# Optimization experiments

Measured on AMD Instinct MI355X. Metric: run time of the kernel, lower is better.

Reference implementation:

```python
import jax, jax.numpy as jnp
import numpy as np

B, T, K, D = 32, 1000, 512, 512


def setup_inputs() -> dict:
    key = jax.random.key(0)
    ks = jax.random.split(key, 10)
    s = lambda k, shape: jax.random.normal(k, shape, jnp.float32) * 0.05
    return {
        "zi": jax.random.randint(ks[0], (B, T), 0, K),
        "c": jax.random.normal(ks[1], (B, D, T), jnp.float32),
        "emb": s(ks[2], (K, D)),
        "W1": s(ks[3], (2 * D, D)), "b1": jnp.zeros((D,), jnp.float32),
        "W2": s(ks[4], (D, D)), "b2": jnp.zeros((D,), jnp.float32),
        "W_ih": s(ks[5], (D, 4 * D)), "b_ih": jnp.zeros((4 * D,), jnp.float32),
        "W_hh": s(ks[6], (D, 4 * D)), "b_hh": jnp.zeros((4 * D,), jnp.float32),
        "W_out": s(ks[7], (D, K)), "b_out": jnp.zeros((K,), jnp.float32),
    }


def reference(zi, c, emb, W1, b1, W2, b2, W_ih, b_ih, W_hh, b_hh, W_out, b_out):
    Bb, Tt = zi.shape
    Dd = emb.shape[1]
    # teacher-forced inputs: embed and shift right by one (pad with zeros)
    z = emb[zi]                                                    # [B,T,D]
    z_prev = jnp.concatenate([jnp.zeros((Bb, 1, Dd), z.dtype), z[:, :-1]], axis=1)
    x = jnp.concatenate([z_prev, jnp.transpose(c, (0, 2, 1))], axis=-1)  # [B,T,2D]
    # prenet has no sequential dependence -> batch over all timesteps
    pre = jax.nn.relu(x @ W1 + b1) @ W2 + b2                       # [B,T,D]
    # precompute the input-to-hidden gate contribution for all steps
    xg = jnp.transpose(pre @ W_ih + b_ih + b_hh, (1, 0, 2))        # [T,B,4D]

    def step(carry, gx):
        h, cc = carry
        gates = gx + h @ W_hh                                      # [B,4D]
        i, f, g, o = jnp.split(gates, 4, axis=-1)                  # torch LSTMCell order
        i = jax.nn.sigmoid(i)
        f = jax.nn.sigmoid(f)
        g = jnp.tanh(g)
        o = jax.nn.sigmoid(o)
        cc = f * cc + i * g
        h = o * jnp.tanh(cc)
        return (h, cc), h

    h0 = jnp.zeros((Bb, Dd), pre.dtype)
    _, hs = jax.lax.scan(step, (h0, h0), xg)                       # [T,B,D]
    logits = hs @ W_out + b_out                                    # [T,B,K]
    return jnp.transpose(logits, (1, 2, 0))                        # [B,K,T]
```

## Files before the change

kernel.cpp:

```cpp
#include <hip/hip_runtime.h>
#include <stdint.h>

typedef unsigned short u16;
typedef unsigned int u32;
typedef unsigned long long u64;
typedef __attribute__((ext_vector_type(8))) short bh8;
typedef __attribute__((ext_vector_type(8))) unsigned short u16x8;
typedef __attribute__((ext_vector_type(4))) float f32x4;

#define B_ 32
#define T_ 1000
#define D_ 512
#define NG 2048

__device__ __forceinline__ float bf2f(u16 u) {
  union { unsigned int i; float f; } v; v.i = ((unsigned int)u) << 16; return v.f;
}
__device__ __forceinline__ u16 f2bf(float f) {
  union { float f; unsigned int i; } v; v.f = f;
  return (u16)((v.i + 0x7fffu + ((v.i >> 16) & 1u)) >> 16);
}

__global__ __launch_bounds__(256) void wtrans_k(const float* __restrict__ src,
                                                u16* __restrict__ dst, int R, int C) {
  __shared__ float tile[32][33];
  const int r0 = blockIdx.x * 32, c0 = blockIdx.y * 32;
  const int tid = threadIdx.x;
#pragma unroll
  for (int q = 0; q < 4; q++) {
    int idx = q * 256 + tid, rr = idx >> 5, cc = idx & 31;
    tile[rr][cc] = src[(size_t)(r0 + rr) * C + c0 + cc];
  }
  __syncthreads();
#pragma unroll
  for (int q = 0; q < 4; q++) {
    int idx = q * 256 + tid, cc = idx >> 5, rr = idx & 31;
    dst[(size_t)(c0 + cc) * R + r0 + rr] = f2bf(tile[rr][cc]);
  }
}

__global__ void bsum_k(const float* __restrict__ a, const float* __restrict__ b,
                       float* __restrict__ o) {
  int i = blockIdx.x * blockDim.x + threadIdx.x;
  if (i < NG) o[i] = a[i] + b[i];
}

__global__ __launch_bounds__(256) void embed_k(const int* __restrict__ zi,
                                               const float* __restrict__ emb,
                                               u16* __restrict__ x) {
  const int tid = threadIdx.x;
  const int r = blockIdx.x * 4 + (tid >> 6);
  const int d0 = (tid & 63) * 8;
  const int t = r >> 5, b = r & 31;
  u16x8 o;
  if (t == 0) {
#pragma unroll
    for (int i = 0; i < 8; i++) o[i] = 0;
  } else {
    const int zv = zi[b * T_ + t - 1];
    const float* s = emb + (size_t)zv * D_ + d0;
#pragma unroll
    for (int i = 0; i < 8; i++) o[i] = f2bf(s[i]);
  }
  *(u16x8*)(x + (size_t)r * 1024 + d0) = o;
}

__global__ __launch_bounds__(256) void ctrans_k(const float* __restrict__ c,
                                                u16* __restrict__ x) {
  __shared__ float tile[32][65];
  const int b = blockIdx.z, d0 = blockIdx.y * 32, t0 = blockIdx.x * 64;
  const int tid = threadIdx.x;
  const int dd = tid >> 3, tt0 = (tid & 7) * 8;
  const float* src = c + ((size_t)b * D_ + d0 + dd) * T_ + t0 + tt0;
#pragma unroll
  for (int i = 0; i < 8; i++) {
    int tt = tt0 + i;
    tile[dd][tt] = (t0 + tt < T_) ? src[i] : 0.f;
  }
  __syncthreads();
  const int tt = tid & 63, dq = tid >> 6;
  if (t0 + tt < T_) {
    u16x8 o;
#pragma unroll
    for (int i = 0; i < 8; i++) o[i] = f2bf(tile[dq * 8 + i][tt]);
    *(u16x8*)(x + ((size_t)(t0 + tt) * 32 + b) * 1024 + 512 + d0 + dq * 8) = o;
  }
}

template <bool RELU, bool SCATTER>
__global__ __launch_bounds__(256, 2) void gemm_k(const u16* __restrict__ A,
                                                 const u16* __restrict__ Bt,
                                                 const float* __restrict__ bias,
                                                 void* __restrict__ Cout,
                                                 int M, int N, int K) {
  __shared__ u16 Al[128 * 40];
  __shared__ u16 Bl[128 * 40];
  const int tid = threadIdx.x;
  const int w = tid >> 6, l = tid & 63;
  const int row0 = blockIdx.x * 128, col0 = blockIdx.y * 128;
  const int wr = (w >> 1) * 64, wc = (w & 1) * 64;
  f32x4 acc[4][4];
  const f32x4 zero = {0.f, 0.f, 0.f, 0.f};
#pragma unroll
  for (int i = 0; i < 4; i++)
#pragma unroll
    for (int j = 0; j < 4; j++) acc[i][j] = zero;

  const int sm = tid >> 2;
  const int sk = (tid & 3) * 8;
  const u16* Ap = A + (size_t)(row0 + sm) * K + sk;
  const u16* Bp = Bt + (size_t)(col0 + sm) * K + sk;
  const size_t half = (size_t)64 * K;
  const int ldo = sm * 40 + sk;
  const int lr = l & 15, lk = (l >> 4) * 8;
  const int KT = K >> 5;

  bh8 a0 = *(const bh8*)Ap, a1 = *(const bh8*)(Ap + half);
  bh8 b0 = *(const bh8*)Bp, b1 = *(const bh8*)(Bp + half);

  for (int kt = 0; kt < KT; kt++) {
    const int kn = (kt + 1 < KT) ? (kt + 1) * 32 : 0;
    bh8 na0 = *(const bh8*)(Ap + kn), na1 = *(const bh8*)(Ap + half + kn);
    bh8 nb0 = *(const bh8*)(Bp + kn), nb1 = *(const bh8*)(Bp + half + kn);
    *(bh8*)(Al + ldo) = a0;
    *(bh8*)(Al + ldo + 64 * 40) = a1;
    *(bh8*)(Bl + ldo) = b0;
    *(bh8*)(Bl + ldo + 64 * 40) = b1;
    __syncthreads();
    bh8 af[4], bfr[4];
#pragma unroll
    for (int i = 0; i < 4; i++) af[i] = *(const bh8*)(Al + (wr + i * 16 + lr) * 40 + lk);
#pragma unroll
    for (int j = 0; j < 4; j++) bfr[j] = *(const bh8*)(Bl + (wc + j * 16 + lr) * 40 + lk);
#pragma unroll
    for (int i = 0; i < 4; i++)
#pragma unroll
      for (int j = 0; j < 4; j++)
        acc[i][j] = __builtin_amdgcn_mfma_f32_16x16x32_bf16(af[i], bfr[j], acc[i][j], 0, 0, 0);
    __syncthreads();
    a0 = na0; a1 = na1; b0 = nb0; b1 = nb1;
  }

  const int lrow = (l >> 4) * 4;
#pragma unroll
  for (int j = 0; j < 4; j++) {
    const int n = col0 + wc + j * 16 + lr;
    const float bv = bias[n];
#pragma unroll
    for (int i = 0; i < 4; i++) {
      const int r = row0 + wr + i * 16 + lrow;
      if (SCATTER) {
        const int bb = r / T_;
        const int t = r - bb * T_;
        f32x4 o;
#pragma unroll
        for (int e = 0; e < 4; e++) o[e] = acc[i][j][e] + bv;
        *(f32x4*)((float*)Cout + ((size_t)bb * N + n) * T_ + t) = o;
      } else {
#pragma unroll
        for (int e = 0; e < 4; e++) {
          float v = acc[i][j][e] + bv;
          if (RELU) v = v > 0.f ? v : 0.f;
          ((u16*)Cout)[(size_t)(r + e) * N + n] = f2bf(v);
        }
      }
    }
  }
}

__device__ __forceinline__ void poll8(const u32* p, u64 q[8], bool slow) {
  const u64 a = (u64)(uintptr_t)p;
  if (!slow) {
    asm volatile(
        "global_load_dwordx2 %0, %8, off sc0\n\t"
        "global_load_dwordx2 %1, %8, off offset:256 sc0\n\t"
        "global_load_dwordx2 %2, %8, off offset:512 sc0\n\t"
        "global_load_dwordx2 %3, %8, off offset:768 sc0\n\t"
        "global_load_dwordx2 %4, %8, off offset:1024 sc0\n\t"
        "global_load_dwordx2 %5, %8, off offset:1280 sc0\n\t"
        "global_load_dwordx2 %6, %8, off offset:1536 sc0\n\t"
        "global_load_dwordx2 %7, %8, off offset:1792 sc0\n\t"
        "s_waitcnt vmcnt(0)"
        : "=&v"(q[0]), "=&v"(q[1]), "=&v"(q[2]), "=&v"(q[3]),
          "=&v"(q[4]), "=&v"(q[5]), "=&v"(q[6]), "=&v"(q[7])
        : "v"(a)
        : "memory");
  } else {
    asm volatile(
        "global_load_dwordx2 %0, %8, off sc1\n\t"
        "global_load_dwordx2 %1, %8, off offset:256 sc1\n\t"
        "global_load_dwordx2 %2, %8, off offset:512 sc1\n\t"
        "global_load_dwordx2 %3, %8, off offset:768 sc1\n\t"
        "global_load_dwordx2 %4, %8, off offset:1024 sc1\n\t"
        "global_load_dwordx2 %5, %8, off offset:1280 sc1\n\t"
        "global_load_dwordx2 %6, %8, off offset:1536 sc1\n\t"
        "global_load_dwordx2 %7, %8, off offset:1792 sc1\n\t"
        "s_waitcnt vmcnt(0)"
        : "=&v"(q[0]), "=&v"(q[1]), "=&v"(q[2]), "=&v"(q[3]),
          "=&v"(q[4]), "=&v"(q[5]), "=&v"(q[6]), "=&v"(q[7])
        : "v"(a)
        : "memory");
  }
}

__global__ __launch_bounds__(256, 1) void scan_k(const u16* __restrict__ xg,
                                                 const u16* __restrict__ Whht,
                                                 u16* __restrict__ hs,
                                                 u32* hbuf) {
  __shared__ u16 hstage[16 * 512];
  __shared__ float gl[4][68];
  const int tid = threadIdx.x;
  const int wgid = blockIdx.x;
  const int grp = wgid & 7;
  const int wgin = wgid >> 3;
  const int D0 = wgin * 16;
  const int w = tid >> 6, l = tid & 63;
  const int lr = l & 15, lc = l >> 4;

  u32* fb = hbuf;
  u32* sb = hbuf + 32768;

  bh8 bfr[16];
  {
    const u16* wp = Whht + (size_t)(w * 512 + D0 + lr) * 512 + lc * 8;
#pragma unroll
    for (int kk = 0; kk < 16; kk++) bfr[kk] = *(const bh8*)(wp + kk * 32);
  }

  for (int i = tid; i < 16 * 256; i += 256) ((u32*)hstage)[i] = 0u;

  const int pb = l >> 4, pd = l & 15;
  const int gbat = grp * 4 + pb;
  float ccv = 0.f;
  u16 xh[4];
  if (w == 0) {
    const u16* xp = xg + (size_t)gbat * NG + D0 + pd;
#pragma unroll
    for (int g = 0; g < 4; g++) xh[g] = xp[g * 512];
  }
  const int rb = (w - 2) * 2 + (l >> 5);
  const int l5 = l & 31;
  bool slowmode = false;
  __syncthreads();

  for (int t = 0; t < T_; t++) {
    f32x4 e0 = {0.f, 0.f, 0.f, 0.f}, e1 = e0;
#pragma unroll
    for (int kk = 0; kk < 16; kk += 2) {
      bh8 af0 = *(const bh8*)(hstage + (kk + 0) * 512 + l * 8);
      bh8 af1 = *(const bh8*)(hstage + (kk + 1) * 512 + l * 8);
      e0 = __builtin_amdgcn_mfma_f32_16x16x32_bf16(af0, bfr[kk + 0], e0, 0, 0, 0);
      e1 = __builtin_amdgcn_mfma_f32_16x16x32_bf16(af1, bfr[kk + 1], e1, 0, 0, 0);
    }
    const f32x4 acc = e0 + e1;
    if (lc == 0) {
#pragma unroll
      for (int e = 0; e < 4; e++) gl[e][w * 16 + lr] = acc[e];
    }
    asm volatile("s_waitcnt lgkmcnt(0)\n\ts_barrier" ::: "memory");
    __builtin_amdgcn_sched_barrier(0);

    if (w == 0) {
      const float gi = gl[pb][ 0 + pd] + bf2f(xh[0]);
      const float gf = gl[pb][16 + pd] + bf2f(xh[1]);
      const float gg = gl[pb][32 + pd] + bf2f(xh[2]);
      const float go = gl[pb][48 + pd] + bf2f(xh[3]);
      const float si = 1.f / (1.f + __expf(-gi));
      const float sf = 1.f / (1.f + __expf(-gf));
      const float tg = 1.f - 2.f / (__expf(2.f * gg) + 1.f);
      const float so = 1.f / (1.f + __expf(-go));
      ccv = sf * ccv + si * tg;
      const float hv = so * (1.f - 2.f / (__expf(2.f * ccv) + 1.f));
      const u16 hb = f2bf(hv);
      if (t + 1 < T_) {
        const u32 tagged = ((u32)(t + 1) << 16) | (u32)hb;
        const size_t idx = ((size_t)((t & 1) * 8 + grp) * 4 + pb) * 512 + D0 + pd;
        asm volatile("global_store_dword %0, %1, off sc0"
                     :: "v"((u64)(uintptr_t)(fb + idx)), "v"(tagged) : "memory");
        (void)__hip_atomic_exchange(sb + idx, tagged, __ATOMIC_RELAXED,
                                    __HIP_MEMORY_SCOPE_AGENT);
      }
      hs[((size_t)gbat * T_ + t) * 512 + D0 + pd] = hb;
      if (t + 1 < T_) {
        const u16* xp = xg + ((size_t)(t + 1) * 32 + gbat) * NG + D0 + pd;
#pragma unroll
        for (int g = 0; g < 4; g++) xh[g] = xp[g * 512];
      }
    } else if (w >= 2 && t + 1 < T_) {
      const u32 tag = (u32)(t + 1);
      const size_t base = ((size_t)((t & 1) * 8 + grp) * 4 + rb) * 512 + 2 * l5;
      u64 q[8];
      int rounds = 0;
      for (;;) {
        poll8(fb + base, q, false);
        if (slowmode) poll8(sb + base, q, true);
        u32 bad = 0;
#pragma unroll
        for (int s = 0; s < 8; s++) {
          bad |= ((u32)q[s] >> 16) ^ tag;
          bad |= ((u32)(q[s] >> 32) >> 16) ^ tag;
        }
        if (!__ballot(bad != 0u)) break;
        if (++rounds > 256) slowmode = true;
      }
#pragma unroll
      for (int s = 0; s < 8; s++) {
        const int k = 2 * l5 + 64 * s;
        const u32 wv = ((u32)q[s] & 0xffffu) | ((u32)(q[s] >> 32) << 16);
        *(u32*)(hstage + (k >> 5) * 512 + (rb + ((k >> 3) & 3) * 16) * 8 + (k & 7)) = wv;
      }
    }
    asm volatile("s_waitcnt lgkmcnt(0)\n\ts_barrier" ::: "memory");
    __builtin_amdgcn_sched_barrier(0);
  }
}

extern "C" void kernel_launch(void* const* d_in, const int* in_sizes, int n_in,
                              void* d_out, int out_size, void* d_ws, size_t ws_size,
                              hipStream_t stream) {
  const int*   zi    = (const int*)d_in[0];
  const float* c     = (const float*)d_in[1];
  const float* emb   = (const float*)d_in[2];
  const float* W1    = (const float*)d_in[3];
  const float* b1    = (const float*)d_in[4];
  const float* W2    = (const float*)d_in[5];
  const float* b2    = (const float*)d_in[6];
  const float* W_ih  = (const float*)d_in[7];
  const float* b_ih  = (const float*)d_in[8];
  const float* W_hh  = (const float*)d_in[9];
  const float* b_hh  = (const float*)d_in[10];
  const float* W_out = (const float*)d_in[11];
  const float* b_out = (const float*)d_in[12];
  float* out = (float*)d_out;
  char* ws = (char*)d_ws;

  const size_t x_off   = 0;
  const size_t xg_off  = 65536000;
  const size_t pre_off = 32768000;
  const size_t w_off   = xg_off + 131072000;
  u16* xb    = (u16*)(ws + x_off);
  u16* hsb   = (u16*)(ws + x_off);
  u16* preb  = (u16*)(ws + pre_off);
  u16* xgb   = (u16*)(ws + xg_off);
  u16* h1b   = (u16*)(ws + xg_off);
  u16* W1t   = (u16*)(ws + w_off);
  u16* W2t   = W1t + 512 * 1024;
  u16* Wiht  = W2t + 512 * 512;
  u16* Whht  = Wiht + 2048 * 512;
  u16* Woutt = Whht + 2048 * 512;
  float* bsum = (float*)(Woutt + 512 * 512);
  u32* hbuf  = (u32*)(bsum + NG);

  hipMemsetAsync(hbuf, 0, 2 * 2 * 8 * 4 * 512 * sizeof(u32), stream);

  wtrans_k<<<dim3(32, 16), 256, 0, stream>>>(W1, W1t, 1024, 512);
  wtrans_k<<<dim3(16, 16), 256, 0, stream>>>(W2, W2t, 512, 512);
  wtrans_k<<<dim3(16, 64), 256, 0, stream>>>(W_ih, Wiht, 512, 2048);
  wtrans_k<<<dim3(16, 64), 256, 0, stream>>>(W_hh, Whht, 512, 2048);
  wtrans_k<<<dim3(16, 16), 256, 0, stream>>>(W_out, Woutt, 512, 512);
  bsum_k<<<8, 256, 0, stream>>>(b_ih, b_hh, bsum);
  embed_k<<<8000, 256, 0, stream>>>(zi, emb, xb);
  ctrans_k<<<dim3(16, 16, 32), 256, 0, stream>>>(c, xb);

  gemm_k<true,  false><<<dim3(250, 4),  256, 0, stream>>>(xb,   W1t,   b1,    h1b,  32000, 512,  1024);
  gemm_k<false, false><<<dim3(250, 4),  256, 0, stream>>>(h1b,  W2t,   b2,    preb, 32000, 512,  512);
  gemm_k<false, false><<<dim3(250, 16), 256, 0, stream>>>(preb, Wiht,  bsum,  xgb,  32000, 2048, 512);
  scan_k<<<256, 256, 0, stream>>>(xgb, Whht, hsb, hbuf);
  gemm_k<false, true ><<<dim3(250, 4),  256, 0, stream>>>(hsb,  Woutt, b_out, out,  32000, 512,  512);
}
```

Before: 3.192 ms.

## Halve scan workgroups, give each 32 hidden dims, poll with all waves

The persistent LSTM scan now runs 128 active workgroups instead of 256. Each one owns 32 hidden dimensions and keeps two sets of W_hh fragments in registers, so every A-fragment load feeds two MFMAs. All four waves poll the exchange buffer with two dwordx4 loads each instead of two waves doing eight dwordx2 loads, and the shared staging buffer is padded to avoid bank conflicts. The slow path now uses atomic loads from the secondary buffer only after a timeout. The aim is fewer participants in the cross-workgroup sync and cheaper polling per step, at the cost of more register pressure and more serial gate work per workgroup.

```diff
diff --git a/kernel.cpp b/kernel.cpp
--- a/kernel.cpp
+++ b/kernel.cpp
@@ -7,6 +7,7 @@
 typedef __attribute__((ext_vector_type(8))) short bh8;
 typedef __attribute__((ext_vector_type(8))) unsigned short u16x8;
 typedef __attribute__((ext_vector_type(4))) float f32x4;
+typedef __attribute__((ext_vector_type(4))) unsigned int u32x4;
 
 #define B_ 32
 #define T_ 1000
@@ -168,146 +169,143 @@
   }
 }
 
-__device__ __forceinline__ void poll8(const u32* p, u64 q[8], bool slow) {
-  const u64 a = (u64)(uintptr_t)p;
-  if (!slow) {
-    asm volatile(
-        "global_load_dwordx2 %0, %8, off sc0\n\t"
-        "global_load_dwordx2 %1, %8, off offset:256 sc0\n\t"
-        "global_load_dwordx2 %2, %8, off offset:512 sc0\n\t"
-        "global_load_dwordx2 %3, %8, off offset:768 sc0\n\t"
-        "global_load_dwordx2 %4, %8, off offset:1024 sc0\n\t"
-        "global_load_dwordx2 %5, %8, off offset:1280 sc0\n\t"
-        "global_load_dwordx2 %6, %8, off offset:1536 sc0\n\t"
-        "global_load_dwordx2 %7, %8, off offset:1792 sc0\n\t"
-        "s_waitcnt vmcnt(0)"
-        : "=&v"(q[0]), "=&v"(q[1]), "=&v"(q[2]), "=&v"(q[3]),
-          "=&v"(q[4]), "=&v"(q[5]), "=&v"(q[6]), "=&v"(q[7])
-        : "v"(a)
-        : "memory");
-  } else {
-    asm volatile(
-        "global_load_dwordx2 %0, %8, off sc1\n\t"
-        "global_load_dwordx2 %1, %8, off offset:256 sc1\n\t"
-        "global_load_dwordx2 %2, %8, off offset:512 sc1\n\t"
-        "global_load_dwordx2 %3, %8, off offset:768 sc1\n\t"
-        "global_load_dwordx2 %4, %8, off offset:1024 sc1\n\t"
-        "global_load_dwordx2 %5, %8, off offset:1280 sc1\n\t"
-        "global_load_dwordx2 %6, %8, off offset:1536 sc1\n\t"
-        "global_load_dwordx2 %7, %8, off offset:1792 sc1\n\t"
-        "s_waitcnt vmcnt(0)"
-        : "=&v"(q[0]), "=&v"(q[1]), "=&v"(q[2]), "=&v"(q[3]),
-          "=&v"(q[4]), "=&v"(q[5]), "=&v"(q[6]), "=&v"(q[7])
-        : "v"(a)
-        : "memory");
-  }
-}
-
 __global__ __launch_bounds__(256, 1) void scan_k(const u16* __restrict__ xg,
                                                  const u16* __restrict__ Whht,
                                                  u16* __restrict__ hs,
                                                  u32* hbuf) {
-  __shared__ u16 hstage[16 * 512];
-  __shared__ float gl[4][68];
+  __shared__ u16 hstage[16 * 552];
+  __shared__ float gl[4 * 132];
   const int tid = threadIdx.x;
   const int wgid = blockIdx.x;
   const int grp = wgid & 7;
   const int wgin = wgid >> 3;
-  const int D0 = wgin * 16;
+  if (wgin >= 16) return;
+  const int D0 = wgin * 32;
   const int w = tid >> 6, l = tid & 63;
   const int lr = l & 15, lc = l >> 4;
+  const int aoff = lc * 136 + lr * 8;
 
   u32* fb = hbuf;
   u32* sb = hbuf + 32768;
 
-  bh8 bfr[16];
-  {
-    const u16* wp = Whht + (size_t)(w * 512 + D0 + lr) * 512 + lc * 8;
-#pragma unroll
-    for (int kk = 0; kk < 16; kk++) bfr[kk] = *(const bh8*)(wp + kk * 32);
-  }
-
-  for (int i = tid; i < 16 * 256; i += 256) ((u32*)hstage)[i] = 0u;
-
-  const int pb = l >> 4, pd = l & 15;
+  bh8 bfr[2][16];
+#pragma unroll
+  for (int j = 0; j < 2; j++) {
+    const int c = w * 512 + D0 + j * 16 + lr;
+    const u16* wp = Whht + (size_t)c * 512 + lc * 8;
+#pragma unroll
+    for (int kk = 0; kk < 16; kk++) bfr[j][kk] = *(const bh8*)(wp + kk * 32);
+  }
+
+  for (int i = tid; i < 16 * 552 / 2; i += 256) ((u32*)hstage)[i] = 0u;
+
+  const int pb = tid >> 5, pd = tid & 31;
   const int gbat = grp * 4 + pb;
+  const int gdim = D0 + pd;
   float ccv = 0.f;
   u16 xh[4];
-  if (w == 0) {
-    const u16* xp = xg + (size_t)gbat * NG + D0 + pd;
+  if (tid < 128) {
+    const u16* xp = xg + (size_t)gbat * NG + gdim;
 #pragma unroll
     for (int g = 0; g < 4; g++) xh[g] = xp[g * 512];
   }
-  const int rb = (w - 2) * 2 + (l >> 5);
-  const int l5 = l & 31;
+  const int rb = tid >> 6;
+  const int rd0 = (tid & 63) * 8;
+  const int stidx = (rd0 >> 5) * 552 + ((rd0 >> 3) & 3) * 136 + rb * 8;
   bool slowmode = false;
   __syncthreads();
 
   for (int t = 0; t < T_; t++) {
-    f32x4 e0 = {0.f, 0.f, 0.f, 0.f}, e1 = e0;
-#pragma unroll
-    for (int kk = 0; kk < 16; kk += 2) {
-      bh8 af0 = *(const bh8*)(hstage + (kk + 0) * 512 + l * 8);
-      bh8 af1 = *(const bh8*)(hstage + (kk + 1) * 512 + l * 8);
-      e0 = __builtin_amdgcn_mfma_f32_16x16x32_bf16(af0, bfr[kk + 0], e0, 0, 0, 0);
-      e1 = __builtin_amdgcn_mfma_f32_16x16x32_bf16(af1, bfr[kk + 1], e1, 0, 0, 0);
-    }
-    const f32x4 acc = e0 + e1;
+    f32x4 a0 = {0.f, 0.f, 0.f, 0.f}, a1 = a0;
+#pragma unroll
+    for (int kk = 0; kk < 16; kk++) {
+      bh8 af = *(const bh8*)(hstage + kk * 552 + aoff);
+      a0 = __builtin_amdgcn_mfma_f32_16x16x32_bf16(af, bfr[0][kk], a0, 0, 0, 0);
+      a1 = __builtin_amdgcn_mfma_f32_16x16x32_bf16(af, bfr[1][kk], a1, 0, 0, 0);
+    }
     if (lc == 0) {
 #pragma unroll
-      for (int e = 0; e < 4; e++) gl[e][w * 16 + lr] = acc[e];
+      for (int e = 0; e < 4; e++) {
+        gl[e * 132 + w * 32 + lr] = a0[e];
+        gl[e * 132 + w * 32 + 16 + lr] = a1[e];
+      }
     }
     asm volatile("s_waitcnt lgkmcnt(0)\n\ts_barrier" ::: "memory");
     __builtin_amdgcn_sched_barrier(0);
 
-    if (w == 0) {
-      const float gi = gl[pb][ 0 + pd] + bf2f(xh[0]);
-      const float gf = gl[pb][16 + pd] + bf2f(xh[1]);
-      const float gg = gl[pb][32 + pd] + bf2f(xh[2]);
-      const float go = gl[pb][48 + pd] + bf2f(xh[3]);
+    u16 hb = 0;
+    if (tid < 128) {
+      const float gi = gl[pb * 132 + pd]      + bf2f(xh[0]);
+      const float gf = gl[pb * 132 + 32 + pd] + bf2f(xh[1]);
+      const float gg = gl[pb * 132 + 64 + pd] + bf2f(xh[2]);
+      const float go = gl[pb * 132 + 96 + pd] + bf2f(xh[3]);
       const float si = 1.f / (1.f + __expf(-gi));
       const float sf = 1.f / (1.f + __expf(-gf));
       const float tg = 1.f - 2.f / (__expf(2.f * gg) + 1.f);
       const float so = 1.f / (1.f + __expf(-go));
       ccv = sf * ccv + si * tg;
       const float hv = so * (1.f - 2.f / (__expf(2.f * ccv) + 1.f));
-      const u16 hb = f2bf(hv);
+      hb = f2bf(hv);
       if (t + 1 < T_) {
         const u32 tagged = ((u32)(t + 1) << 16) | (u32)hb;
-        const size_t idx = ((size_t)((t & 1) * 8 + grp) * 4 + pb) * 512 + D0 + pd;
+        const size_t idx = ((size_t)((t & 1) * 8 + grp) * 4 + pb) * 512 + gdim;
         asm volatile("global_store_dword %0, %1, off sc0"
                      :: "v"((u64)(uintptr_t)(fb + idx)), "v"(tagged) : "memory");
         (void)__hip_atomic_exchange(sb + idx, tagged, __ATOMIC_RELAXED,
                                     __HIP_MEMORY_SCOPE_AGENT);
       }
-      hs[((size_t)gbat * T_ + t) * 512 + D0 + pd] = hb;
+    }
+    if (t + 1 < T_) {
+      const u32 tag = (u32)(t + 1);
+      const size_t base = ((size_t)((t & 1) * 8 + grp) * 4 + rb) * 512 + rd0;
+      const u64 pa = (u64)(uintptr_t)(fb + base);
+      u32x4 qa, qb;
+      if (!slowmode) {
+        int rounds = 0;
+        for (;;) {
+          asm volatile("global_load_dwordx4 %0, %2, off sc0\n\t"
+                       "global_load_dwordx4 %1, %2, off offset:16 sc0\n\t"
+                       "s_waitcnt vmcnt(0)"
+                       : "=&v"(qa), "=&v"(qb) : "v"(pa) : "memory");
+          const bool bad = (qa[0] >> 16) != tag || (qa[1] >> 16) != tag ||
+                           (qa[2] >> 16) != tag || (qa[3] >> 16) != tag ||
+                           (qb[0] >> 16) != tag || (qb[1] >> 16) != tag ||
+                           (qb[2] >> 16) != tag || (qb[3] >> 16) != tag;
+          if (!__ballot(bad)) break;
+          if (++rounds > 512) { slowmode = true; break; }
+        }
+      }
+      if (slowmode) {
+        const u64* sp = (const u64*)(sb + base);
+        for (;;) {
+          u64 s0 = __hip_atomic_load(sp + 0, __ATOMIC_RELAXED, __HIP_MEMORY_SCOPE_AGENT);
+          u64 s1 = __hip_atomic_load(sp + 1, __ATOMIC_RELAXED, __HIP_MEMORY_SCOPE_AGENT);
+          u64 s2 = __hip_atomic_load(sp + 2, __ATOMIC_RELAXED, __HIP_MEMORY_SCOPE_AGENT);
+          u64 s3 = __hip_atomic_load(sp + 3, __ATOMIC_RELAXED, __HIP_MEMORY_SCOPE_AGENT);
+          qa[0] = (u32)s0; qa[1] = (u32)(s0 >> 32);
+          qa[2] = (u32)s1; qa[3] = (u32)(s1 >> 32);
+          qb[0] = (u32)s2; qb[1] = (u32)(s2 >> 32);
+          qb[2] = (u32)s3; qb[3] = (u32)(s3 >> 32);
+          const bool bad = (qa[0] >> 16) != tag || (qa[1] >> 16) != tag ||
+                           (qa[2] >> 16) != tag || (qa[3] >> 16) != tag ||
+                           (qb[0] >> 16) != tag || (qb[1] >> 16) != tag ||
+                           (qb[2] >> 16) != tag || (qb[3] >> 16) != tag;
+          if (!__ballot(bad)) break;
+        }
+      }
+      u32x4 pw;
+      pw[0] = (qa[0] & 0xffffu) | (qa[1] << 16);
+      pw[1] = (qa[2] & 0xffffu) | (qa[3] << 16);
+      pw[2] = (qb[0] & 0xffffu) | (qb[1] << 16);
+      pw[3] = (qb[2] & 0xffffu) | (qb[3] << 16);
+      *(u32x4*)(hstage + stidx) = pw;
+    }
+    if (tid < 128) {
+      hs[((size_t)gbat * T_ + t) * 512 + gdim] = hb;
       if (t + 1 < T_) {
-        const u16* xp = xg + ((size_t)(t + 1) * 32 + gbat) * NG + D0 + pd;
+        const u16* xp = xg + ((size_t)(t + 1) * 32 + gbat) * NG + gdim;
 #pragma unroll
         for (int g = 0; g < 4; g++) xh[g] = xp[g * 512];
-      }
-    } else if (w >= 2 && t + 1 < T_) {
-      const u32 tag = (u32)(t + 1);
-      const size_t base = ((size_t)((t & 1) * 8 + grp) * 4 + rb) * 512 + 2 * l5;
-      u64 q[8];
-      int rounds = 0;
-      for (;;) {
-        poll8(fb + base, q, false);
-        if (slowmode) poll8(sb + base, q, true);
-        u32 bad = 0;
-#pragma unroll
-        for (int s = 0; s < 8; s++) {
-          bad |= ((u32)q[s] >> 16) ^ tag;
-          bad |= ((u32)(q[s] >> 32) >> 16) ^ tag;
-        }
-        if (!__ballot(bad != 0u)) break;
-        if (++rounds > 256) slowmode = true;
-      }
-#pragma unroll
-      for (int s = 0; s < 8; s++) {
-        const int k = 2 * l5 + 64 * s;
-        const u32 wv = ((u32)q[s] & 0xffffu) | ((u32)(q[s] >> 32) << 16);
-        *(u32*)(hstage + (k >> 5) * 512 + (rb + ((k >> 3) & 3) * 16) * 8 + (k & 7)) = wv;
       }
     }
     asm volatile("s_waitcnt lgkmcnt(0)\n\ts_barrier" ::: "memory");
@@ -351,7 +349,7 @@
   float* bsum = (float*)(Woutt + 512 * 512);
   u32* hbuf  = (u32*)(bsum + NG);
 
-  hipMemsetAsync(hbuf, 0, 2 * 2 * 8 * 4 * 512 * sizeof(u32), stream);
+  hipMemsetAsync(hbuf, 0, 2 * 32768 * sizeof(u32), stream);
 
   wtrans_k<<<dim3(32, 16), 256, 0, stream>>>(W1, W1t, 1024, 512);
   wtrans_k<<<dim3(16, 16), 256, 0, stream>>>(W2, W2t, 512, 512);
```

Result: faster. 2.970 ms (-7.0%).
